# Kernel optimization log

Measured on AMD Instinct MI355X. Metric: run time of the kernel, lower is better.

Reference implementation:

```python
import jax, jax.numpy as jnp
import numpy as np

B, D_W, D_C, D_P = 4096, 2048, 1024, 2048
RANK = D_W // 4  # 512, per A_U/A_V shapes (d_w, d_w//4)


def setup_inputs() -> dict:
    key = jax.random.key(0)
    ks = jax.random.split(key, 10)
    return {
        "w_prev": jax.random.normal(ks[0], (B, D_W), jnp.float32),
        "z_t": jax.random.normal(ks[1], (B, D_P), jnp.float32),
        "c_t": jax.random.normal(ks[2], (B, D_C), jnp.float32),
        # params (mirroring flax init: A_diag zeros, A_U/A_V normal(0.01),
        # Dense kernels lecun_normal-ish scale, zero biases)
        "A_diag": jnp.zeros((D_W,), jnp.float32),
        "A_U": 0.01 * jax.random.normal(ks[3], (D_W, RANK), jnp.float32),
        "A_V": 0.01 * jax.random.normal(ks[4], (D_W, RANK), jnp.float32),
        "W_mod": jax.random.normal(ks[5], (D_C, D_W), jnp.float32) / np.sqrt(D_C),
        "b_mod": jnp.zeros((D_W,), jnp.float32),
        "W_B": jax.random.normal(ks[6], (D_C + D_P, D_W), jnp.float32) / np.sqrt(D_C + D_P),
        "b_B": jnp.zeros((D_W,), jnp.float32),
    }


def reference(w_prev, z_t, c_t, A_diag, A_U, A_V, W_mod, b_mod, W_B, b_B):
    # A = diag(tanh(A_diag)*0.9) + A_U @ A_V^T, row-scaled by modulation.
    # Equivalent (same math) without materializing [B, d_w, d_w]:
    #   (A * m[:, :, None]) @ w = m * (a_diag * w + A_U @ (A_V^T @ w))
    a_diag = jnp.tanh(A_diag) * 0.9                              # [d_w]
    modulation = jnp.tanh(c_t @ W_mod + b_mod)                   # [B, d_w]
    Aw = a_diag * w_prev + (w_prev @ A_V) @ A_U.T                # [B, d_w]
    Bt = jnp.concatenate([c_t, z_t], axis=-1) @ W_B + b_B        # [B, d_w]
    return modulation * Aw + Bt
```

## Files before the change

kernel.cpp:

```cpp
#include <hip/hip_runtime.h>


#define DEV __device__ __forceinline__

typedef __bf16 v8bf __attribute__((ext_vector_type(8)));
typedef __bf16 v4bf __attribute__((ext_vector_type(4)));
typedef float  v4f  __attribute__((ext_vector_type(4)));

typedef __attribute__((address_space(1))) const unsigned int* as1_cuint_ptr;
typedef __attribute__((address_space(3))) unsigned int*       as3_uint_ptr;

DEV void async16(const void* g, void* l) {
  __builtin_amdgcn_global_load_lds(
      (as1_cuint_ptr)(unsigned long long)g,
      (as3_uint_ptr)(unsigned long long)l,
      16, 0, 0);
}

DEV float tanh_fast(float x) {
  x = fminf(15.f, fmaxf(-15.f, x));
  float e = __expf(2.f * x);
  return (e - 1.f) / (e + 1.f);
}


__global__ void cvt_f32_bf16(const float* __restrict__ src,
                             __bf16* __restrict__ dst, int n) {
  int i = (blockIdx.x * 256 + threadIdx.x) * 4;
  if (i + 3 < n) {
    float4 v = *reinterpret_cast<const float4*>(src + i);
    v4bf o;
    o.x = (__bf16)v.x; o.y = (__bf16)v.y; o.z = (__bf16)v.z; o.w = (__bf16)v.w;
    *reinterpret_cast<v4bf*>(dst + i) = o;
  }
}

__global__ void transpose_cvt(const float* __restrict__ src,
                              __bf16* __restrict__ dst, int R, int C) {
  __shared__ float t[32][33];
  const int c0 = blockIdx.x * 32, r0 = blockIdx.y * 32;
  const int tx = threadIdx.x & 31, ty = threadIdx.x >> 5;
#pragma unroll
  for (int rr = 0; rr < 32; rr += 8)
    t[ty + rr][tx] = src[(size_t)(r0 + ty + rr) * C + c0 + tx];
  __syncthreads();
#pragma unroll
  for (int rr = 0; rr < 32; rr += 8)
    dst[(size_t)(c0 + ty + rr) * R + r0 + tx] = (__bf16)t[tx][ty + rr];
}

__global__ void adiag_kernel(const float* __restrict__ A_diag,
                             float* __restrict__ out, int n) {
  int i = blockIdx.x * 256 + threadIdx.x;
  if (i < n) out[i] = tanh_fast(A_diag[i]) * 0.9f;
}

template <int MODE, bool SPLIT>
__global__ __launch_bounds__(256, 2) void gemm_bf16_k(
    const __bf16* __restrict__ A0, int lda0, int kswitch,
    const __bf16* __restrict__ A1, int lda1,
    const __bf16* __restrict__ Bt, int ldb,
    int M, int N, int K,
    void* __restrict__ outp,
    const float* __restrict__ bias,
    const __bf16* __restrict__ modp,
    const __bf16* __restrict__ alrp,
    const float* __restrict__ wprev,
    const float* __restrict__ adiag) {
  __shared__ __align__(16) __bf16 As[128 * 32];
  __shared__ __align__(16) __bf16 Bs[128 * 32];

  const int tid  = threadIdx.x;
  const int lane = tid & 63;
  const int wid  = tid >> 6;
  const int wm   = wid >> 1;
  const int wn   = wid & 1;
  const int l16  = lane & 15;
  const int quad = lane >> 4;

  const int m0 = blockIdx.y * 128;
  const int n0 = blockIdx.x * 128;

  const int sg_row = lane >> 2;
  const int sg_k   = (lane & 3) * 8;

  v4f acc[4][4];
#pragma unroll
  for (int i = 0; i < 4; ++i)
#pragma unroll
    for (int j = 0; j < 4; ++j) {
      v4f z = {0.f, 0.f, 0.f, 0.f};
      acc[i][j] = z;
    }

  for (int k0 = 0; k0 < K; k0 += 32) {
    __syncthreads();
#pragma unroll
    for (int t = 0; t < 2; ++t) {
      const int chunk = wid * 2 + t;
      const int row   = chunk * 16 + sg_row;
      const __bf16* gA;
      if (!SPLIT || k0 < kswitch)
        gA = A0 + (size_t)(m0 + row) * lda0 + (k0 + sg_k);
      else
        gA = A1 + (size_t)(m0 + row) * lda1 + (k0 - kswitch + sg_k);
      async16((const void*)gA, (void*)&As[chunk * 512 + lane * 8]);
      const __bf16* gB = Bt + (size_t)(n0 + row) * ldb + (k0 + sg_k);
      async16((const void*)gB, (void*)&Bs[chunk * 512 + lane * 8]);
    }
    __syncthreads();

    const v8bf* Ap = reinterpret_cast<const v8bf*>(As);
    const v8bf* Bp = reinterpret_cast<const v8bf*>(Bs);
    v8bf a[4], b[4];
#pragma unroll
    for (int i = 0; i < 4; ++i) a[i] = Ap[(wm * 64 + i * 16 + l16) * 4 + quad];
#pragma unroll
    for (int j = 0; j < 4; ++j) b[j] = Bp[(wn * 64 + j * 16 + l16) * 4 + quad];
#pragma unroll
    for (int i = 0; i < 4; ++i)
#pragma unroll
      for (int j = 0; j < 4; ++j)
        acc[i][j] = __builtin_amdgcn_mfma_f32_16x16x32_bf16(a[i], b[j],
                                                            acc[i][j], 0, 0, 0);
  }

  const int mBase = m0 + wm * 64 + quad * 4;
  const int nBase = n0 + wn * 64 + l16;

  if (MODE == 0) {
    __bf16* out = (__bf16*)outp;
#pragma unroll
    for (int j = 0; j < 4; ++j) {
      const int n = nBase + j * 16;
#pragma unroll
      for (int i = 0; i < 4; ++i)
#pragma unroll
        for (int r = 0; r < 4; ++r) {
          const int m = mBase + i * 16 + r;
          out[(size_t)m * N + n] = (__bf16)acc[i][j][r];
        }
    }
  } else if (MODE == 1) {
    __bf16* out = (__bf16*)outp;
#pragma unroll
    for (int j = 0; j < 4; ++j) {
      const int n  = nBase + j * 16;
      const float bn = bias[n];
#pragma unroll
      for (int i = 0; i < 4; ++i)
#pragma unroll
        for (int r = 0; r < 4; ++r) {
          const int m = mBase + i * 16 + r;
          out[(size_t)m * N + n] = (__bf16)tanh_fast(acc[i][j][r] + bn);
        }
    }
  } else {
    float* out = (float*)outp;
#pragma unroll
    for (int j = 0; j < 4; ++j) {
      const int n  = nBase + j * 16;
      const float bn = bias[n];
      const float ad = adiag[n];
#pragma unroll
      for (int i = 0; i < 4; ++i)
#pragma unroll
        for (int r = 0; r < 4; ++r) {
          const int m   = mBase + i * 16 + r;
          const size_t idx = (size_t)m * N + n;
          const float md = (float)modp[idx];
          const float al = (float)alrp[idx];
          out[idx] = md * (ad * wprev[idx] + al) + acc[i][j][r] + bn;
        }
    }
  }
}


extern "C" void kernel_launch(void* const* d_in, const int* in_sizes, int n_in,
                              void* d_out, int out_size, void* d_ws,
                              size_t ws_size, hipStream_t stream) {
  const float* w_prev = (const float*)d_in[0];
  const float* z_t    = (const float*)d_in[1];
  const float* c_t    = (const float*)d_in[2];
  const float* A_diag = (const float*)d_in[3];
  const float* A_U    = (const float*)d_in[4];
  const float* A_V    = (const float*)d_in[5];
  const float* W_mod  = (const float*)d_in[6];
  const float* b_mod  = (const float*)d_in[7];
  const float* W_B    = (const float*)d_in[8];
  const float* b_B    = (const float*)d_in[9];

  constexpr int Bsz = 4096, DW = 2048, DC = 1024, DP = 2048, RK = 512;
  const size_t MB = 1ull << 20;
  char* ws = (char*)d_ws;
  __bf16* w_bf   = (__bf16*)(ws + 0);
  __bf16* z_bf   = (__bf16*)(ws + 16 * MB);
  __bf16* c_bf   = (__bf16*)(ws + 32 * MB);
  __bf16* AU_bf  = (__bf16*)(ws + 40 * MB);
  __bf16* AVt    = (__bf16*)(ws + 42 * MB);
  __bf16* Wmodt  = (__bf16*)(ws + 44 * MB);
  __bf16* WBt    = (__bf16*)(ws + 48 * MB);
  __bf16* P_bf   = (__bf16*)(ws + 60 * MB);
  __bf16* mod_bf = (__bf16*)(ws + 64 * MB);
  __bf16* alr_bf = (__bf16*)(ws + 0);
  float*  adiag  = (float*)(ws + 80 * MB);

  cvt_f32_bf16<<<(Bsz * DW) / 1024, 256, 0, stream>>>(w_prev, w_bf, Bsz * DW);
  cvt_f32_bf16<<<(Bsz * DP) / 1024, 256, 0, stream>>>(z_t, z_bf, Bsz * DP);
  cvt_f32_bf16<<<(Bsz * DC) / 1024, 256, 0, stream>>>(c_t, c_bf, Bsz * DC);
  cvt_f32_bf16<<<(DW * RK) / 1024, 256, 0, stream>>>(A_U, AU_bf, DW * RK);
  transpose_cvt<<<dim3(RK / 32, DW / 32), 256, 0, stream>>>(A_V, AVt, DW, RK);
  transpose_cvt<<<dim3(DW / 32, DC / 32), 256, 0, stream>>>(W_mod, Wmodt, DC, DW);
  transpose_cvt<<<dim3(DW / 32, (DC + DP) / 32), 256, 0, stream>>>(W_B, WBt,
                                                                   DC + DP, DW);
  adiag_kernel<<<DW / 256, 256, 0, stream>>>(A_diag, adiag, DW);

  gemm_bf16_k<0, false><<<dim3(RK / 128, Bsz / 128), 256, 0, stream>>>(
      w_bf, DW, 0, w_bf, DW, AVt, DW, Bsz, RK, DW, (void*)P_bf,
      nullptr, nullptr, nullptr, nullptr, nullptr);

  gemm_bf16_k<1, false><<<dim3(DW / 128, Bsz / 128), 256, 0, stream>>>(
      c_bf, DC, 0, c_bf, DC, Wmodt, DC, Bsz, DW, DC, (void*)mod_bf,
      b_mod, nullptr, nullptr, nullptr, nullptr);

  gemm_bf16_k<0, false><<<dim3(DW / 128, Bsz / 128), 256, 0, stream>>>(
      P_bf, RK, 0, P_bf, RK, AU_bf, RK, Bsz, DW, RK, (void*)alr_bf,
      nullptr, nullptr, nullptr, nullptr, nullptr);

  gemm_bf16_k<2, true><<<dim3(DW / 128, Bsz / 128), 256, 0, stream>>>(
      c_bf, DC, DC, z_bf, DP, WBt, DC + DP, Bsz, DW, DC + DP, d_out,
      b_B, mod_bf, alr_bf, w_prev, adiag);
}
```

Measured before the change: 350.8 us.

## Precompute dense A matrix and fuse all GEMMs into one kernel

Materialises M = diag(a) + A_U·A_V^T as a 2048x2048 bf16 matrix with a small GEMM. A single fused kernel then accumulates c·W_mod, applies tanh in registers, accumulates w·M^T, scales by the modulation and adds the c/z·W_B contribution before writing fp32 output. This removes the intermediate mod/alr/P buffers, their global round trips, the fp32 w_prev reread and several launches. In exchange the low-rank path becomes a full-rank K=2048 GEMM, which adds roughly a quarter more total FLOPs. Keeping the modulation values in registers across phases also raises register pressure.

```diff
diff --git a/kernel.cpp b/kernel.cpp
--- a/kernel.cpp
+++ b/kernel.cpp
@@ -55,61 +55,35 @@
   if (i < n) out[i] = tanh_fast(A_diag[i]) * 0.9f;
 }
 
-template <int MODE, bool SPLIT>
-__global__ __launch_bounds__(256, 2) void gemm_bf16_k(
-    const __bf16* __restrict__ A0, int lda0, int kswitch,
-    const __bf16* __restrict__ A1, int lda1,
-    const __bf16* __restrict__ Bt, int ldb,
-    int M, int N, int K,
-    void* __restrict__ outp,
-    const float* __restrict__ bias,
-    const __bf16* __restrict__ modp,
-    const __bf16* __restrict__ alrp,
-    const float* __restrict__ wprev,
-    const float* __restrict__ adiag) {
+__global__ __launch_bounds__(256, 2) void gemm_mt(
+    const __bf16* __restrict__ A0, const __bf16* __restrict__ Bt,
+    int N, int K, __bf16* __restrict__ out, const float* __restrict__ adiag) {
   __shared__ __align__(16) __bf16 As[128 * 32];
   __shared__ __align__(16) __bf16 Bs[128 * 32];
 
-  const int tid  = threadIdx.x;
-  const int lane = tid & 63;
-  const int wid  = tid >> 6;
-  const int wm   = wid >> 1;
-  const int wn   = wid & 1;
-  const int l16  = lane & 15;
-  const int quad = lane >> 4;
-
-  const int m0 = blockIdx.y * 128;
-  const int n0 = blockIdx.x * 128;
-
-  const int sg_row = lane >> 2;
-  const int sg_k   = (lane & 3) * 8;
+  const int tid = threadIdx.x, lane = tid & 63, wid = tid >> 6;
+  const int wm = wid >> 1, wn = wid & 1, l16 = lane & 15, quad = lane >> 4;
+  const int m0 = blockIdx.y * 128, n0 = blockIdx.x * 128;
+  const int sg_row = lane >> 2, sg_k = (lane & 3) * 8;
 
   v4f acc[4][4];
 #pragma unroll
   for (int i = 0; i < 4; ++i)
 #pragma unroll
-    for (int j = 0; j < 4; ++j) {
-      v4f z = {0.f, 0.f, 0.f, 0.f};
-      acc[i][j] = z;
-    }
+    for (int j = 0; j < 4; ++j) { v4f zz = {0,0,0,0}; acc[i][j] = zz; }
 
   for (int k0 = 0; k0 < K; k0 += 32) {
     __syncthreads();
 #pragma unroll
     for (int t = 0; t < 2; ++t) {
       const int chunk = wid * 2 + t;
-      const int row   = chunk * 16 + sg_row;
-      const __bf16* gA;
-      if (!SPLIT || k0 < kswitch)
-        gA = A0 + (size_t)(m0 + row) * lda0 + (k0 + sg_k);
-      else
-        gA = A1 + (size_t)(m0 + row) * lda1 + (k0 - kswitch + sg_k);
-      async16((const void*)gA, (void*)&As[chunk * 512 + lane * 8]);
-      const __bf16* gB = Bt + (size_t)(n0 + row) * ldb + (k0 + sg_k);
-      async16((const void*)gB, (void*)&Bs[chunk * 512 + lane * 8]);
+      const int row = chunk * 16 + sg_row;
+      async16((const void*)(A0 + (size_t)(m0 + row) * K + k0 + sg_k),
+              (void*)&As[chunk * 512 + lane * 8]);
+      async16((const void*)(Bt + (size_t)(n0 + row) * K + k0 + sg_k),
+              (void*)&Bs[chunk * 512 + lane * 8]);
     }
     __syncthreads();
-
     const v8bf* Ap = reinterpret_cast<const v8bf*>(As);
     const v8bf* Bp = reinterpret_cast<const v8bf*>(Bs);
     v8bf a[4], b[4];
@@ -127,52 +101,114 @@
 
   const int mBase = m0 + wm * 64 + quad * 4;
   const int nBase = n0 + wn * 64 + l16;
-
-  if (MODE == 0) {
-    __bf16* out = (__bf16*)outp;
-#pragma unroll
-    for (int j = 0; j < 4; ++j) {
-      const int n = nBase + j * 16;
-#pragma unroll
-      for (int i = 0; i < 4; ++i)
-#pragma unroll
-        for (int r = 0; r < 4; ++r) {
-          const int m = mBase + i * 16 + r;
-          out[(size_t)m * N + n] = (__bf16)acc[i][j][r];
-        }
+#pragma unroll
+  for (int j = 0; j < 4; ++j) {
+    const int n = nBase + j * 16;
+#pragma unroll
+    for (int i = 0; i < 4; ++i)
+#pragma unroll
+      for (int r = 0; r < 4; ++r) {
+        const int m = mBase + i * 16 + r;
+        float v = acc[i][j][r];
+        if (m == n) v += adiag[m];
+        out[(size_t)m * N + n] = (__bf16)v;
+      }
+  }
+}
+
+__global__ __launch_bounds__(256, 2) void fused_main(
+    const __bf16* __restrict__ c, const __bf16* __restrict__ z,
+    const __bf16* __restrict__ w, const __bf16* __restrict__ Wmodt,
+    const __bf16* __restrict__ Mt, const __bf16* __restrict__ WBt,
+    const float* __restrict__ b_mod, const float* __restrict__ b_B,
+    float* __restrict__ out) {
+  constexpr int DC = 1024, DW = 2048, KB = 3072;
+  __shared__ __align__(16) __bf16 As[128 * 32];
+  __shared__ __align__(16) __bf16 Bs[128 * 32];
+
+  const int tid = threadIdx.x, lane = tid & 63, wid = tid >> 6;
+  const int wm = wid >> 1, wn = wid & 1, l16 = lane & 15, quad = lane >> 4;
+  const int m0 = blockIdx.y * 128;
+  const int n0 = blockIdx.x * 128;
+  const int sg_row = lane >> 2, sg_k = (lane & 3) * 8;
+  const int ldsA = (wid * 2) * 512 + lane * 8;
+  const int ldsA2 = (wid * 2 + 1) * 512 + lane * 8;
+  const int rowA = (wid * 2) * 16 + sg_row;
+  const int rowA2 = (wid * 2 + 1) * 16 + sg_row;
+
+  v4f acc[4][4];
+#pragma unroll
+  for (int i = 0; i < 4; ++i)
+#pragma unroll
+    for (int j = 0; j < 4; ++j) { v4f zz = {0,0,0,0}; acc[i][j] = zz; }
+
+  auto kstep = [&](const __bf16* gA, size_t lda, const __bf16* gB, size_t ldb,
+                   int kA, int kB) {
+    __syncthreads();
+    async16((const void*)(gA + (size_t)(m0 + rowA) * lda + kA + sg_k),
+            (void*)&As[ldsA]);
+    async16((const void*)(gB + (size_t)(n0 + rowA) * ldb + kB + sg_k),
+            (void*)&Bs[ldsA]);
+    async16((const void*)(gA + (size_t)(m0 + rowA2) * lda + kA + sg_k),
+            (void*)&As[ldsA2]);
+    async16((const void*)(gB + (size_t)(n0 + rowA2) * ldb + kB + sg_k),
+            (void*)&Bs[ldsA2]);
+    __syncthreads();
+    const v8bf* Ap = reinterpret_cast<const v8bf*>(As);
+    const v8bf* Bp = reinterpret_cast<const v8bf*>(Bs);
+    v8bf a[4], b[4];
+#pragma unroll
+    for (int i = 0; i < 4; ++i) a[i] = Ap[(wm * 64 + i * 16 + l16) * 4 + quad];
+#pragma unroll
+    for (int j = 0; j < 4; ++j) b[j] = Bp[(wn * 64 + j * 16 + l16) * 4 + quad];
+#pragma unroll
+    for (int i = 0; i < 4; ++i)
+#pragma unroll
+      for (int j = 0; j < 4; ++j)
+        acc[i][j] = __builtin_amdgcn_mfma_f32_16x16x32_bf16(a[i], b[j],
+                                                            acc[i][j], 0, 0, 0);
+  };
+
+  const int nBase = n0 + wn * 64 + l16;
+
+  for (int k0 = 0; k0 < DC; k0 += 32) kstep(c, DC, Wmodt, DC, k0, k0);
+
+  v4f mod_s[4][4];
+#pragma unroll
+  for (int j = 0; j < 4; ++j) {
+    const float bn = b_mod[nBase + j * 16];
+#pragma unroll
+    for (int i = 0; i < 4; ++i) {
+#pragma unroll
+      for (int r = 0; r < 4; ++r)
+        mod_s[i][j][r] = tanh_fast(acc[i][j][r] + bn);
+      v4f zz = {0,0,0,0};
+      acc[i][j] = zz;
     }
-  } else if (MODE == 1) {
-    __bf16* out = (__bf16*)outp;
-#pragma unroll
-    for (int j = 0; j < 4; ++j) {
-      const int n  = nBase + j * 16;
-      const float bn = bias[n];
-#pragma unroll
-      for (int i = 0; i < 4; ++i)
-#pragma unroll
-        for (int r = 0; r < 4; ++r) {
-          const int m = mBase + i * 16 + r;
-          out[(size_t)m * N + n] = (__bf16)tanh_fast(acc[i][j][r] + bn);
-        }
-    }
-  } else {
-    float* out = (float*)outp;
-#pragma unroll
-    for (int j = 0; j < 4; ++j) {
-      const int n  = nBase + j * 16;
-      const float bn = bias[n];
-      const float ad = adiag[n];
-#pragma unroll
-      for (int i = 0; i < 4; ++i)
-#pragma unroll
-        for (int r = 0; r < 4; ++r) {
-          const int m   = mBase + i * 16 + r;
-          const size_t idx = (size_t)m * N + n;
-          const float md = (float)modp[idx];
-          const float al = (float)alrp[idx];
-          out[idx] = md * (ad * wprev[idx] + al) + acc[i][j][r] + bn;
-        }
-    }
+  }
+
+  for (int k0 = 0; k0 < DW; k0 += 32) kstep(w, DW, Mt, DW, k0, k0);
+
+#pragma unroll
+  for (int i = 0; i < 4; ++i)
+#pragma unroll
+    for (int j = 0; j < 4; ++j) acc[i][j] *= mod_s[i][j];
+
+  for (int k0 = 0; k0 < DC; k0 += 32) kstep(c, DC, WBt, KB, k0, k0);
+  for (int k0 = DC; k0 < KB; k0 += 32) kstep(z, DW, WBt, KB, k0 - DC, k0);
+
+  const int mBase = m0 + wm * 64 + quad * 4;
+#pragma unroll
+  for (int j = 0; j < 4; ++j) {
+    const int n = nBase + j * 16;
+    const float bn = b_B[n];
+#pragma unroll
+    for (int i = 0; i < 4; ++i)
+#pragma unroll
+      for (int r = 0; r < 4; ++r) {
+        const int m = mBase + i * 16 + r;
+        out[(size_t)m * DW + n] = acc[i][j][r] + bn;
+      }
   }
 }
 
@@ -194,41 +230,29 @@
   constexpr int Bsz = 4096, DW = 2048, DC = 1024, DP = 2048, RK = 512;
   const size_t MB = 1ull << 20;
   char* ws = (char*)d_ws;
-  __bf16* w_bf   = (__bf16*)(ws + 0);
-  __bf16* z_bf   = (__bf16*)(ws + 16 * MB);
-  __bf16* c_bf   = (__bf16*)(ws + 32 * MB);
-  __bf16* AU_bf  = (__bf16*)(ws + 40 * MB);
-  __bf16* AVt    = (__bf16*)(ws + 42 * MB);
-  __bf16* Wmodt  = (__bf16*)(ws + 44 * MB);
-  __bf16* WBt    = (__bf16*)(ws + 48 * MB);
-  __bf16* P_bf   = (__bf16*)(ws + 60 * MB);
-  __bf16* mod_bf = (__bf16*)(ws + 64 * MB);
-  __bf16* alr_bf = (__bf16*)(ws + 0);
-  float*  adiag  = (float*)(ws + 80 * MB);
+  __bf16* w_bf  = (__bf16*)(ws + 0);
+  __bf16* z_bf  = (__bf16*)(ws + 16 * MB);
+  __bf16* c_bf  = (__bf16*)(ws + 32 * MB);
+  __bf16* AU_bf = (__bf16*)(ws + 40 * MB);
+  __bf16* AV_bf = (__bf16*)(ws + 42 * MB);
+  __bf16* Wmodt = (__bf16*)(ws + 44 * MB);
+  __bf16* WBt   = (__bf16*)(ws + 48 * MB);
+  __bf16* Mt    = (__bf16*)(ws + 60 * MB);
+  float*  adiag = (float*)(ws + 68 * MB);
 
   cvt_f32_bf16<<<(Bsz * DW) / 1024, 256, 0, stream>>>(w_prev, w_bf, Bsz * DW);
   cvt_f32_bf16<<<(Bsz * DP) / 1024, 256, 0, stream>>>(z_t, z_bf, Bsz * DP);
   cvt_f32_bf16<<<(Bsz * DC) / 1024, 256, 0, stream>>>(c_t, c_bf, Bsz * DC);
   cvt_f32_bf16<<<(DW * RK) / 1024, 256, 0, stream>>>(A_U, AU_bf, DW * RK);
-  transpose_cvt<<<dim3(RK / 32, DW / 32), 256, 0, stream>>>(A_V, AVt, DW, RK);
+  cvt_f32_bf16<<<(DW * RK) / 1024, 256, 0, stream>>>(A_V, AV_bf, DW * RK);
   transpose_cvt<<<dim3(DW / 32, DC / 32), 256, 0, stream>>>(W_mod, Wmodt, DC, DW);
   transpose_cvt<<<dim3(DW / 32, (DC + DP) / 32), 256, 0, stream>>>(W_B, WBt,
                                                                    DC + DP, DW);
   adiag_kernel<<<DW / 256, 256, 0, stream>>>(A_diag, adiag, DW);
 
-  gemm_bf16_k<0, false><<<dim3(RK / 128, Bsz / 128), 256, 0, stream>>>(
-      w_bf, DW, 0, w_bf, DW, AVt, DW, Bsz, RK, DW, (void*)P_bf,
-      nullptr, nullptr, nullptr, nullptr, nullptr);
-
-  gemm_bf16_k<1, false><<<dim3(DW / 128, Bsz / 128), 256, 0, stream>>>(
-      c_bf, DC, 0, c_bf, DC, Wmodt, DC, Bsz, DW, DC, (void*)mod_bf,
-      b_mod, nullptr, nullptr, nullptr, nullptr);
-
-  gemm_bf16_k<0, false><<<dim3(DW / 128, Bsz / 128), 256, 0, stream>>>(
-      P_bf, RK, 0, P_bf, RK, AU_bf, RK, Bsz, DW, RK, (void*)alr_bf,
-      nullptr, nullptr, nullptr, nullptr, nullptr);
-
-  gemm_bf16_k<2, true><<<dim3(DW / 128, Bsz / 128), 256, 0, stream>>>(
-      c_bf, DC, DC, z_bf, DP, WBt, DC + DP, Bsz, DW, DC + DP, d_out,
-      b_B, mod_bf, alr_bf, w_prev, adiag);
-}
+  gemm_mt<<<dim3(DW / 128, DW / 128), 256, 0, stream>>>(AU_bf, AV_bf, DW, RK,
+                                                        Mt, adiag);
+
+  fused_main<<<dim3(DW / 128, Bsz / 128), 256, 0, stream>>>(
+      c_bf, z_bf, w_bf, Wmodt, Mt, WBt, b_mod, b_B, (float*)d_out);
+}
```

Measured after the change: 334.0 us. 4.8% less time.
